# Kernel tuning notes

Hardware: AMD Instinct MI355X
Metric: run time of the kernel (lower is better)

## Reference

```python
import jax, jax.numpy as jnp
import numpy as np


def setup_inputs() -> dict:
    key = jax.random.key(0)
    ks = jax.random.split(key, 6)
    B, S, I, H, O = 64, 2048, 256, 256, 256
    x = jax.random.normal(ks[0], (B, S, I), dtype=jnp.float32)
    # nn.Linear stores weight as [out_features, in_features]; y = x @ W.T
    W_ih = jax.random.normal(ks[1], (H, I), dtype=jnp.float32) / np.sqrt(I)
    W_hh = jax.random.normal(ks[2], (H, H), dtype=jnp.float32) / np.sqrt(H)
    b_h = jnp.zeros((H,), dtype=jnp.float32)
    W_ho = jax.random.normal(ks[3], (O, H), dtype=jnp.float32) / np.sqrt(H)
    b_o = jax.random.normal(ks[4], (O,), dtype=jnp.float32) / np.sqrt(H)
    return {"x": x, "W_ih": W_ih, "W_hh": W_hh, "b_h": b_h, "W_ho": W_ho, "b_o": b_o}


def reference(x, W_ih, W_hh, b_h, W_ho, b_o):
    B, S, I = x.shape
    H = W_hh.shape[0]
    # Precompute input projection for all timesteps in one GEMM: [B,S,H]
    xW = jnp.einsum('bsi,hi->bsh', x, W_ih) + b_h

    def step(h, xw_t):
        h = jnp.tanh(xw_t + h @ W_hh.T)  # [B,H]
        out = h @ W_ho.T + b_o           # [B,O]
        return h, out

    h0 = jnp.zeros((B, H), dtype=x.dtype)
    # scan over time axis: move S to leading dim
    h_final, outs = jax.lax.scan(step, h0, jnp.swapaxes(xW, 0, 1))
    outputs = jnp.swapaxes(outs, 0, 1)  # [B,S,O]
    return (outputs, h_final)
```

## Files before the change

kernel.cpp:

```cpp
#include <hip/hip_runtime.h>
#include <hip/hip_bf16.h>

#define Bdim 64
#define Sdim 2048
#define Hdim 256

typedef __attribute__((ext_vector_type(8))) short short8;
typedef __attribute__((ext_vector_type(4))) float f32x4;

static __device__ __forceinline__ unsigned short f2bf(float f) {
  union { float f; unsigned int u; } v; v.f = f;
  unsigned int r = v.u + 0x7fffu + ((v.u >> 16) & 1u);
  return (unsigned short)(r >> 16);
}
static __device__ __forceinline__ float bf2f(unsigned short u) {
  union { unsigned int u; float f; } v; v.u = ((unsigned int)u) << 16;
  return v.f;
}
static __device__ __forceinline__ float bflo(unsigned int u) {
  union { unsigned int u; float f; } v; v.u = u << 16; return v.f;
}
static __device__ __forceinline__ float bfhi(unsigned int u) {
  union { unsigned int u; float f; } v; v.u = u & 0xffff0000u; return v.f;
}

#if __has_builtin(__builtin_amdgcn_rcpf)
#define FAST_RCP(x) __builtin_amdgcn_rcpf(x)
#else
#define FAST_RCP(x) (1.0f / (x))
#endif

static __device__ __forceinline__ float tanh_fast(float x) {
  float e = exp2f(x * 2.8853900817779268f);
  return 1.0f - 2.0f * FAST_RCP(1.0f + e);
}

template<int XW_F32>
__global__ __launch_bounds__(256, 1) void rnn_scan_mfma(
    const void* __restrict__ xwp, const float* __restrict__ Whh,
    float* __restrict__ hout, float* __restrict__ hfin) {
  __shared__ __align__(16) unsigned short hbuf[2][16 * 256];
  const int tid = threadIdx.x;
  const int lane = tid & 63;
  const int wv = tid >> 6;
  const int l15 = lane & 15;
  const int g = lane >> 4;
  const int bs = blockIdx.x * 16;

  for (int i = tid; i < 16 * 256; i += 256) hbuf[0][i] = 0;

  short8 wfrag[4][8];
#pragma unroll
  for (int tau = 0; tau < 4; ++tau) {
    int n = wv * 64 + tau * 16 + l15;
#pragma unroll
    for (int ks = 0; ks < 8; ++ks) {
      int k0 = ks * 32 + g * 8;
      const float* p = Whh + n * 256 + k0;
      short8 v;
#pragma unroll
      for (int e = 0; e < 8; ++e) v[e] = (short)f2bf(p[e]);
      wfrag[tau][ks] = v;
    }
  }

  int aroff[8];
#pragma unroll
  for (int ks = 0; ks < 8; ++ks)
    aroff[ks] = l15 * 512 + ((ks * 64 + g * 16) ^ ((l15 & 7) << 4));

  int nb[4], wo[4];
#pragma unroll
  for (int tau = 0; tau < 4; ++tau) {
    nb[tau] = wv * 64 + tau * 16 + g * 4;
    wo[tau] = l15 * 512 + ((2 * nb[tau]) ^ ((l15 & 7) << 4));
  }
  const long rowbase = (long)(bs + l15) * Sdim * Hdim;

  const float* xwf = (const float*)xwp;
  const unsigned short* xwh = (const unsigned short*)xwp;

  auto ldxw = [&](long idx) -> f32x4 {
    if (XW_F32) return *(const f32x4*)(xwf + idx);
    ushort4 a = *(const ushort4*)(xwh + idx);
    f32x4 r; r[0]=bf2f(a.x); r[1]=bf2f(a.y); r[2]=bf2f(a.z); r[3]=bf2f(a.w);
    return r;
  };

  f32x4 bufA[4], bufB[4];
#pragma unroll
  for (int tau = 0; tau < 4; ++tau) {
    bufA[tau] = ldxw(rowbase + nb[tau]);
    bufB[tau] = ldxw(rowbase + Hdim + nb[tau]);
  }

  __syncthreads();

  int cb = 0;
  auto step = [&](int tc, f32x4 (&buf)[4]) {
    f32x4 acc[4];
#pragma unroll
    for (int tau = 0; tau < 4; ++tau) acc[tau] = buf[tau];

    const long tn = (tc + 2 < Sdim) ? tc + 2 : Sdim - 1;
#pragma unroll
    for (int tau = 0; tau < 4; ++tau)
      buf[tau] = ldxw(rowbase + tn * Hdim + nb[tau]);

    const char* hb = (const char*)hbuf[cb];
#pragma unroll
    for (int ks = 0; ks < 8; ++ks) {
      short8 h8 = *(const short8*)(hb + aroff[ks]);
#pragma unroll
      for (int tau = 0; tau < 4; ++tau)
        acc[tau] = __builtin_amdgcn_mfma_f32_16x16x32_bf16(wfrag[tau][ks], h8, acc[tau], 0, 0, 0);
    }

    char* hn = (char*)hbuf[cb ^ 1];
    const long ob = rowbase + (long)tc * Hdim;
#pragma unroll
    for (int tau = 0; tau < 4; ++tau) {
      f32x4 v;
#pragma unroll
      for (int e = 0; e < 4; ++e) v[e] = tanh_fast(acc[tau][e]);
      unsigned int plo, phi;
      asm("v_cvt_pk_bf16_f32 %0, %1, %2" : "=v"(plo) : "v"(v[0]), "v"(v[1]));
      asm("v_cvt_pk_bf16_f32 %0, %1, %2" : "=v"(phi) : "v"(v[2]), "v"(v[3]));
      *(uint2*)(hn + wo[tau]) = make_uint2(plo, phi);
      *(f32x4*)(hout + ob + nb[tau]) = v;
      if (tc == Sdim - 1) *(f32x4*)(hfin + (bs + l15) * Hdim + nb[tau]) = v;
    }

    __builtin_amdgcn_sched_barrier(0);
    asm volatile("s_waitcnt lgkmcnt(0)" ::: "memory");
    __builtin_amdgcn_s_barrier();
    __builtin_amdgcn_sched_barrier(0);
    cb ^= 1;
  };

  for (int t = 0; t < Sdim; t += 2) {
    step(t, bufA);
    step(t + 1, bufB);
  }
}

__global__ __launch_bounds__(256, 1) void rnn_scan_valu_fused(
    const float* __restrict__ x, const float* __restrict__ Wih,
    const float* __restrict__ bh, const float* __restrict__ Whh,
    float* __restrict__ hout, float* __restrict__ hfin) {
  __shared__ __align__(16) uint2 wt[64][256];
  __shared__ __align__(16) float hl[256];
  const int n = threadIdx.x;
  const int b = blockIdx.x;
  {
    const float2* src = (const float2*)Whh;
    unsigned int* w32 = (unsigned int*)wt;
    for (int i = n; i < 32768; i += 256) {
      float2 f = src[i];
      unsigned int u = (unsigned int)f2bf(f.x) | ((unsigned int)f2bf(f.y) << 16);
      int row = i >> 7, kk = i & 127, k4 = kk >> 1, half = kk & 1;
      w32[k4 * 512 + row * 2 + half] = u;
    }
  }
  hl[n] = 0.0f;
  __syncthreads();
  const long base = (long)b * Sdim * Hdim + n;
  for (int t = 0; t < Sdim; ++t) {
    const float* xr = x + ((long)b * Sdim + t) * 256;
    const float* wr = Wih + n * 256;
    float acc = bh[n];
    for (int k = 0; k < 256; ++k) acc += xr[k] * wr[k];
#pragma unroll 8
    for (int k4 = 0; k4 < 64; ++k4) {
      uint2 w2 = wt[k4][n];
      float4 h4 = *(const float4*)&hl[k4 * 4];
      acc += bflo(w2.x) * h4.x + bfhi(w2.x) * h4.y
           + bflo(w2.y) * h4.z + bfhi(w2.y) * h4.w;
    }
    float hv = tanh_fast(acc);
    __syncthreads();
    hl[n] = hv;
    hout[base + (long)t * Hdim] = hv;
    if (t == Sdim - 1) hfin[b * Hdim + n] = hv;
    __syncthreads();
  }
}

template<int A_F32, int OUT_F32>
__global__ __launch_bounds__(512, 2) void gemm256(const void* __restrict__ Ap,
                                                  const float* __restrict__ Wf,
                                                  const float* __restrict__ bias,
                                                  void* __restrict__ outp) {
  __shared__ __align__(16) char wl[131072];
  const int tid = threadIdx.x;
  const int lane = tid & 63;
  const int wv = tid >> 6;
  const int l15 = lane & 15;
  const int g = lane >> 4;
  const long r0 = (long)blockIdx.x * 128;

  for (int i = tid; i < 256 * 64; i += 512) {
    int n = i >> 6;
    int kc = (i & 63) * 4;
    f32x4 c = *(const f32x4*)(Wf + n * 256 + kc);
    unsigned int lo = (unsigned int)f2bf(c[0]) | ((unsigned int)f2bf(c[1]) << 16);
    unsigned int hi = (unsigned int)f2bf(c[2]) | ((unsigned int)f2bf(c[3]) << 16);
    int kb = (kc * 2) ^ ((n & 7) << 4);
    unsigned int* dst = (unsigned int*)(wl + n * 512 + kb);
    dst[0] = lo; dst[1] = hi;
  }
  __syncthreads();

  f32x4 acc[16];
#pragma unroll
  for (int tau = 0; tau < 16; ++tau) {
    float bv = bias[tau * 16 + l15];
    acc[tau][0] = bv; acc[tau][1] = bv; acc[tau][2] = bv; acc[tau][3] = bv;
  }

  const long arow = r0 + wv * 16 + l15;
#pragma unroll
  for (int ks = 0; ks < 8; ++ks) {
    const int k0 = ks * 32 + g * 8;
    short8 a;
    if (A_F32) {
      const f32x4* ap = (const f32x4*)((const float*)Ap + arow * 256 + k0);
      f32x4 x0 = ap[0], x1 = ap[1];
#pragma unroll
      for (int e = 0; e < 4; ++e) { a[e] = (short)f2bf(x0[e]); a[4 + e] = (short)f2bf(x1[e]); }
    } else {
      a = *(const short8*)((const unsigned short*)Ap + arow * 256 + k0);
    }
#pragma unroll
    for (int tau = 0; tau < 16; ++tau) {
      int n = tau * 16 + l15;
      int kb = (k0 * 2) ^ ((n & 7) << 4);
      short8 b = *(const short8*)(wl + n * 512 + kb);
      acc[tau] = __builtin_amdgcn_mfma_f32_16x16x32_bf16(a, b, acc[tau], 0, 0, 0);
    }
  }

#pragma unroll
  for (int tau = 0; tau < 16; ++tau) {
    int n = tau * 16 + l15;
#pragma unroll
    for (int e = 0; e < 4; ++e) {
      long row = r0 + wv * 16 + g * 4 + e;
      if (OUT_F32) ((float*)outp)[row * 256 + n] = acc[tau][e];
      else         ((unsigned short*)outp)[row * 256 + n] = f2bf(acc[tau][e]);
    }
  }
}

extern "C" void kernel_launch(void* const* d_in, const int* in_sizes, int n_in,
                              void* d_out, int out_size, void* d_ws, size_t ws_size,
                              hipStream_t stream) {
  const float* x    = (const float*)d_in[0];
  const float* W_ih = (const float*)d_in[1];
  const float* W_hh = (const float*)d_in[2];
  const float* b_h  = (const float*)d_in[3];
  const float* W_ho = (const float*)d_in[4];
  const float* b_o  = (const float*)d_in[5];
  float* out  = (float*)d_out;
  float* hout = out;
  float* hfin = out + (size_t)Bdim * Sdim * Hdim;

  const int gblocks = (Bdim * Sdim) / 128;
  const size_t need32 = (size_t)Bdim * Sdim * Hdim * 4;
  const size_t need16 = need32 / 2;

  if (ws_size >= need32) {
    gemm256<1, 1><<<gblocks, 512, 0, stream>>>(x, W_ih, b_h, d_ws);
    rnn_scan_mfma<1><<<4, 256, 0, stream>>>(d_ws, W_hh, hout, hfin);
  } else if (ws_size >= need16) {
    gemm256<1, 0><<<gblocks, 512, 0, stream>>>(x, W_ih, b_h, d_ws);
    rnn_scan_mfma<0><<<4, 256, 0, stream>>>(d_ws, W_hh, hout, hfin);
  } else {
    rnn_scan_valu_fused<<<Bdim, 256, 0, stream>>>(x, W_ih, b_h, W_hh, hout, hfin);
  }
  gemm256<1, 1><<<gblocks, 512, 0, stream>>>(hout, W_ho, b_o, out);
}
```

Measured before the change: 2.399 ms.

## Stage xW chunks through LDS and write hidden states as bf16 in workspace

The scan kernel now loads the bf16 input projection in chunks of 4 timesteps with coalesced 16-byte loads into LDS. It uses LDS slots as a 4-deep ring of hidden states and writes the bf16 history back to a workspace buffer, also coalesced, rather than doing per-lane strided fp32 global loads and stores every step. The output GEMM then reads the bf16 hidden states, halving traffic on both ends of the sequential scan. The cost is bf16 rounding of the xW and h histories, plus a larger LDS footprint and a different workspace requirement.

After: 2.872 ms. 1.2x slower.

```diff
diff --git a/kernel.cpp b/kernel.cpp
--- a/kernel.cpp
+++ b/kernel.cpp
@@ -35,11 +35,17 @@
   return 1.0f - 2.0f * FAST_RCP(1.0f + e);
 }
 
-template<int XW_F32>
+#define STEP_BAR() do { __builtin_amdgcn_sched_barrier(0); \
+    asm volatile("s_waitcnt lgkmcnt(0)" ::: "memory"); \
+    __builtin_amdgcn_s_barrier(); \
+    __builtin_amdgcn_sched_barrier(0); } while (0)
+
 __global__ __launch_bounds__(256, 1) void rnn_scan_mfma(
-    const void* __restrict__ xwp, const float* __restrict__ Whh,
-    float* __restrict__ hout, float* __restrict__ hfin) {
-  __shared__ __align__(16) unsigned short hbuf[2][16 * 256];
+    const unsigned short* __restrict__ xw1,
+    const float* __restrict__ Whh,
+    unsigned short* __restrict__ ws2,
+    float* __restrict__ hfin) {
+  __shared__ __align__(16) char lds[65536];
   const int tid = threadIdx.x;
   const int lane = tid & 63;
   const int wv = tid >> 6;
@@ -47,8 +53,6 @@
   const int g = lane >> 4;
   const int bs = blockIdx.x * 16;
 
-  for (int i = tid; i < 16 * 256; i += 256) hbuf[0][i] = 0;
-
   short8 wfrag[4][8];
 #pragma unroll
   for (int tau = 0; tau < 4; ++tau) {
@@ -69,78 +73,103 @@
   for (int ks = 0; ks < 8; ++ks)
     aroff[ks] = l15 * 512 + ((ks * 64 + g * 16) ^ ((l15 & 7) << 4));
 
-  int nb[4], wo[4];
+  int nb[4], wo[4], xo[4];
 #pragma unroll
   for (int tau = 0; tau < 4; ++tau) {
     nb[tau] = wv * 64 + tau * 16 + g * 4;
     wo[tau] = l15 * 512 + ((2 * nb[tau]) ^ ((l15 & 7) << 4));
-  }
-  const long rowbase = (long)(bs + l15) * Sdim * Hdim;
-
-  const float* xwf = (const float*)xwp;
-  const unsigned short* xwh = (const unsigned short*)xwp;
-
-  auto ldxw = [&](long idx) -> f32x4 {
-    if (XW_F32) return *(const f32x4*)(xwf + idx);
-    ushort4 a = *(const ushort4*)(xwh + idx);
-    f32x4 r; r[0]=bf2f(a.x); r[1]=bf2f(a.y); r[2]=bf2f(a.z); r[3]=bf2f(a.w);
-    return r;
-  };
-
-  f32x4 bufA[4], bufB[4];
-#pragma unroll
-  for (int tau = 0; tau < 4; ++tau) {
-    bufA[tau] = ldxw(rowbase + nb[tau]);
-    bufB[tau] = ldxw(rowbase + Hdim + nb[tau]);
-  }
-
-  __syncthreads();
-
-  int cb = 0;
-  auto step = [&](int tc, f32x4 (&buf)[4]) {
-    f32x4 acc[4];
-#pragma unroll
-    for (int tau = 0; tau < 4; ++tau) acc[tau] = buf[tau];
-
-    const long tn = (tc + 2 < Sdim) ? tc + 2 : Sdim - 1;
-#pragma unroll
-    for (int tau = 0; tau < 4; ++tau)
-      buf[tau] = ldxw(rowbase + tn * Hdim + nb[tau]);
-
-    const char* hb = (const char*)hbuf[cb];
-#pragma unroll
-    for (int ks = 0; ks < 8; ++ks) {
-      short8 h8 = *(const short8*)(hb + aroff[ks]);
-#pragma unroll
-      for (int tau = 0; tau < 4; ++tau)
-        acc[tau] = __builtin_amdgcn_mfma_f32_16x16x32_bf16(wfrag[tau][ks], h8, acc[tau], 0, 0, 0);
-    }
-
-    char* hn = (char*)hbuf[cb ^ 1];
-    const long ob = rowbase + (long)tc * Hdim;
-#pragma unroll
-    for (int tau = 0; tau < 4; ++tau) {
-      f32x4 v;
-#pragma unroll
-      for (int e = 0; e < 4; ++e) v[e] = tanh_fast(acc[tau][e]);
-      unsigned int plo, phi;
-      asm("v_cvt_pk_bf16_f32 %0, %1, %2" : "=v"(plo) : "v"(v[0]), "v"(v[1]));
-      asm("v_cvt_pk_bf16_f32 %0, %1, %2" : "=v"(phi) : "v"(v[2]), "v"(v[3]));
-      *(uint2*)(hn + wo[tau]) = make_uint2(plo, phi);
-      *(f32x4*)(hout + ob + nb[tau]) = v;
-      if (tc == Sdim - 1) *(f32x4*)(hfin + (bs + l15) * Hdim + nb[tau]) = v;
-    }
-
-    __builtin_amdgcn_sched_barrier(0);
-    asm volatile("s_waitcnt lgkmcnt(0)" ::: "memory");
-    __builtin_amdgcn_s_barrier();
-    __builtin_amdgcn_sched_barrier(0);
-    cb ^= 1;
-  };
-
-  for (int t = 0; t < Sdim; t += 2) {
-    step(t, bufA);
-    step(t + 1, bufB);
+    xo[tau] = 32768 + l15 * 512 + ((2 * nb[tau]) ^ ((l15 & 7) << 4));
+  }
+
+  {
+    uint4 z; z.x = z.y = z.z = z.w = 0;
+#pragma unroll
+    for (int i = 0; i < 8; ++i) *((uint4*)lds + i * 256 + tid) = z;
+  }
+
+  const int c_n8 = tid & 31, c_ts = (tid >> 5) & 3, c_m0 = tid >> 7;
+  uint4 stg[8];
+
+#pragma unroll
+  for (int it = 0; it < 8; ++it) {
+    int m = c_m0 + it * 2;
+    long e = ((long)(bs + m) * Sdim + c_ts) * Hdim + c_n8 * 8;
+    stg[it] = *(const uint4*)(xw1 + e);
+  }
+
+  for (int C = 0; C < 512; ++C) {
+#pragma unroll
+    for (int it = 0; it < 8; ++it) {
+      int m = c_m0 + it * 2;
+      *(uint4*)(lds + 32768 + c_ts * 8192 + m * 512 + ((c_n8 * 16) ^ ((m & 7) << 4))) = stg[it];
+    }
+    if (C > 0) {
+      const int t0p = (C - 1) * 4;
+#pragma unroll
+      for (int it = 0; it < 8; ++it) {
+        int m = c_m0 + it * 2;
+        uint4 v = *(const uint4*)(lds + c_ts * 8192 + m * 512 + ((c_n8 * 16) ^ ((m & 7) << 4)));
+        long e = ((long)(bs + m) * Sdim + (t0p + c_ts)) * Hdim + c_n8 * 8;
+        *(uint4*)(ws2 + e) = v;
+      }
+    }
+    if (C < 511) {
+      const long t0n = (long)(C + 1) * 4;
+#pragma unroll
+      for (int it = 0; it < 8; ++it) {
+        int m = c_m0 + it * 2;
+        long e = ((long)(bs + m) * Sdim + (t0n + c_ts)) * Hdim + c_n8 * 8;
+        stg[it] = *(const uint4*)(xw1 + e);
+      }
+    }
+    STEP_BAR();
+
+#pragma unroll
+    for (int ts = 0; ts < 4; ++ts) {
+      const int rs = (ts + 3) & 3;
+      const int t = C * 4 + ts;
+
+      f32x4 acc[4];
+#pragma unroll
+      for (int tau = 0; tau < 4; ++tau) {
+        uint2 q = *(const uint2*)(lds + ts * 8192 + xo[tau]);
+        acc[tau][0] = bflo(q.x); acc[tau][1] = bfhi(q.x);
+        acc[tau][2] = bflo(q.y); acc[tau][3] = bfhi(q.y);
+      }
+
+#pragma unroll
+      for (int ks = 0; ks < 8; ++ks) {
+        short8 h8 = *(const short8*)(lds + rs * 8192 + aroff[ks]);
+#pragma unroll
+        for (int tau = 0; tau < 4; ++tau)
+          acc[tau] = __builtin_amdgcn_mfma_f32_16x16x32_bf16(wfrag[tau][ks], h8, acc[tau], 0, 0, 0);
+      }
+
+#pragma unroll
+      for (int tau = 0; tau < 4; ++tau) {
+        f32x4 v;
+#pragma unroll
+        for (int e = 0; e < 4; ++e) v[e] = tanh_fast(acc[tau][e]);
+        unsigned int plo, phi;
+        asm("v_cvt_pk_bf16_f32 %0, %1, %2" : "=v"(plo) : "v"(v[0]), "v"(v[1]));
+        asm("v_cvt_pk_bf16_f32 %0, %1, %2" : "=v"(phi) : "v"(v[2]), "v"(v[3]));
+        *(uint2*)(lds + ts * 8192 + wo[tau]) = make_uint2(plo, phi);
+        if (t == Sdim - 1)
+          *(f32x4*)(hfin + (bs + l15) * Hdim + nb[tau]) = v;
+      }
+      STEP_BAR();
+    }
+  }
+
+  {
+    const int t0p = 511 * 4;
+#pragma unroll
+    for (int it = 0; it < 8; ++it) {
+      int m = c_m0 + it * 2;
+      uint4 v = *(const uint4*)(lds + c_ts * 8192 + m * 512 + ((c_n8 * 16) ^ ((m & 7) << 4)));
+      long e = ((long)(bs + m) * Sdim + (t0p + c_ts)) * Hdim + c_n8 * 8;
+      *(uint4*)(ws2 + e) = v;
+    }
   }
 }
 
@@ -262,21 +291,19 @@
   const float* W_ho = (const float*)d_in[4];
   const float* b_o  = (const float*)d_in[5];
   float* out  = (float*)d_out;
-  float* hout = out;
   float* hfin = out + (size_t)Bdim * Sdim * Hdim;
 
   const int gblocks = (Bdim * Sdim) / 128;
-  const size_t need32 = (size_t)Bdim * Sdim * Hdim * 4;
-  const size_t need16 = need32 / 2;
-
-  if (ws_size >= need32) {
-    gemm256<1, 1><<<gblocks, 512, 0, stream>>>(x, W_ih, b_h, d_ws);
-    rnn_scan_mfma<1><<<4, 256, 0, stream>>>(d_ws, W_hh, hout, hfin);
-  } else if (ws_size >= need16) {
-    gemm256<1, 0><<<gblocks, 512, 0, stream>>>(x, W_ih, b_h, d_ws);
-    rnn_scan_mfma<0><<<4, 256, 0, stream>>>(d_ws, W_hh, hout, hfin);
+  const size_t half = (size_t)Bdim * Sdim * Hdim * 2;
+
+  if (ws_size >= 2 * half) {
+    unsigned short* ws1 = (unsigned short*)d_ws;
+    unsigned short* ws2 = ws1 + (size_t)Bdim * Sdim * Hdim;
+    gemm256<1, 0><<<gblocks, 512, 0, stream>>>(x, W_ih, b_h, ws1);
+    rnn_scan_mfma<<<4, 256, 0, stream>>>(ws1, W_hh, ws2, hfin);
+    gemm256<0, 1><<<gblocks, 512, 0, stream>>>(ws2, W_ho, b_o, out);
   } else {
-    rnn_scan_valu_fused<<<Bdim, 256, 0, stream>>>(x, W_ih, b_h, W_hh, hout, hfin);
-  }
-  gemm256<1, 1><<<gblocks, 512, 0, stream>>>(hout, W_ho, b_o, out);
-}
+    rnn_scan_valu_fused<<<Bdim, 256, 0, stream>>>(x, W_ih, b_h, W_hh, out, hfin);
+    gemm256<1, 1><<<gblocks, 512, 0, stream>>>(out, W_ho, b_o, out);
+  }
+}
```
